# Performance work log

Measured on AMD Instinct MI355X. Metric: run time of the kernel, lower is better.

The kernel has to match this reference:

```python
import jax, jax.numpy as jnp
import numpy as np

B, H, LQ, LK, D = 4, 8, 2048, 2048, 64
FACTOR = 5
SAMPLE_K = min(FACTOR * int(np.ceil(np.log(LK))), LK)  # 40
N_TOP = min(FACTOR * int(np.ceil(np.log(LQ))), LQ)     # 40
SCALE = 1.0 / float(np.sqrt(D))


def setup_inputs() -> dict:
    key = jax.random.key(0)
    kq, kk, kv, ki = jax.random.split(key, 4)
    queries = jax.random.normal(kq, (B, LQ, H, D), dtype=jnp.float32)
    keys = jax.random.normal(kk, (B, LK, H, D), dtype=jnp.float32)
    values = jax.random.normal(kv, (B, LK, H, D), dtype=jnp.float32)
    index_sample = jax.random.randint(ki, (LQ, SAMPLE_K), 0, LK)
    return {"queries": queries, "keys": keys, "values": values,
            "index_sample": index_sample}


def reference(queries, keys, values, index_sample):
    # (B, L, H, D) -> (B, H, L, D)
    Q = queries.transpose(0, 2, 1, 3)
    K = keys.transpose(0, 2, 1, 3)
    V = values.transpose(0, 2, 1, 3)

    # --- _prob_QK: sampled score estimate ---
    # gather sampled keys: (B, H, L_Q, sample_k, D)
    K_sample = K[:, :, index_sample]
    # Q_K_sample: (B, H, L_Q, sample_k)
    qk_sample = jnp.einsum('bhld,bhlsd->bhls', Q, K_sample)
    # sparsity measure M = max - mean over sampled keys
    M = qk_sample.max(axis=-1) - qk_sample.mean(axis=-1)  # (B, H, L_Q)
    _, idx = jax.lax.top_k(M, N_TOP)                      # (B, H, u)

    # exact scores for top queries
    Q_reduce = jnp.take_along_axis(Q, idx[..., None], axis=2)     # (B, H, u, D)
    scores_top = jnp.einsum('bhud,bhkd->bhuk', Q_reduce, K) * SCALE

    # --- initial context (mask_flag=True -> cumulative sum of V) ---
    context = jnp.cumsum(V, axis=2)  # (B, H, L_Q, D)

    # --- update context at top-query positions with exact attention ---
    attn = jax.nn.softmax(scores_top, axis=-1)                    # (B, H, u, L_K)
    context_v = jnp.einsum('bhuk,bhkd->bhud', attn, V)            # (B, H, u, D)
    bi = jnp.arange(B)[:, None, None]
    hi = jnp.arange(H)[None, :, None]
    context = context.at[bi, hi, idx].set(context_v)

    # back to (B, L_Q, H, D); output_attention=False -> attn dropped
    return context.transpose(0, 2, 1, 3)
```

## Files before the change

kernel.cpp:

```cpp
#include <hip/hip_runtime.h>
#include <hip/hip_bf16.h>
#include <math.h>

#define NB 4
#define NH 8
#define SLQ 2048
#define SLK 2048
#define DD 64
#define SK 40
#define NTOP 40
#define SCL 0.125f
#define CH 128
#define NCH (SLK / CH)
#define UB 2
#define NUG (NTOP / UB)
#define NBH (NB * NH)
#define KB 128
#define NKB (SLK / KB)
#define PVU 4
#define NPG (NTOP / PVU)

typedef unsigned short ushort_t;

__device__ __forceinline__ float bf2f(unsigned int u16) {
    union { unsigned int i; float f; } v;
    v.i = u16 << 16;
    return v.f;
}
__device__ __forceinline__ ushort_t f2bf(float f) {
    union { float f; unsigned int i; } v;
    v.f = f;
    unsigned int x = v.i;
    unsigned int r = (x + 0x7FFFu + ((x >> 16) & 1u)) >> 16;
    return (ushort_t)r;
}
template <bool F32>
__device__ __forceinline__ float le(const void* p, size_t i) {
    return F32 ? ((const float*)p)[i] : bf2f(((const ushort_t*)p)[i]);
}
template <bool F32>
__device__ __forceinline__ void se(void* p, size_t i, float v) {
    if (F32) ((float*)p)[i] = v;
    else ((ushort_t*)p)[i] = f2bf(v);
}
template <bool F32>
__device__ __forceinline__ float4 load4(const void* p, size_t off) {
    if (F32) return *(const float4*)((const float*)p + off);
    uint2 u = *(const uint2*)((const ushort_t*)p + off);
    float4 r;
    r.x = bf2f(u.x & 0xffffu); r.y = bf2f(u.x >> 16);
    r.z = bf2f(u.y & 0xffffu); r.w = bf2f(u.y >> 16);
    return r;
}
template <bool F32>
__device__ __forceinline__ void store4(void* p, size_t off, float4 v) {
    if (F32) { *(float4*)((float*)p + off) = v; return; }
    uint2 u;
    u.x = (unsigned)f2bf(v.x) | ((unsigned)f2bf(v.y) << 16);
    u.y = (unsigned)f2bf(v.z) | ((unsigned)f2bf(v.w) << 16);
    *(uint2*)((ushort_t*)p + off) = u;
}
template <bool F32>
__device__ __forceinline__ void load8(const void* p, size_t elem_off, float* r) {
    if (F32) {
        const float4* q = (const float4*)((const float*)p + elem_off);
        float4 a = q[0], b = q[1];
        r[0] = a.x; r[1] = a.y; r[2] = a.z; r[3] = a.w;
        r[4] = b.x; r[5] = b.y; r[6] = b.z; r[7] = b.w;
    } else {
        uint4 u = *(const uint4*)((const ushort_t*)p + elem_off);
        unsigned int w[4] = {u.x, u.y, u.z, u.w};
#pragma unroll
        for (int j = 0; j < 4; j++) {
            r[2 * j + 0] = bf2f(w[j] & 0xffffu);
            r[2 * j + 1] = bf2f(w[j] >> 16);
        }
    }
}

__global__ void k_probe(const unsigned int* __restrict__ qw, int* __restrict__ flag)
{
    int t = threadIdx.x;
    unsigned int w = qw[t * 37];
    int cnt = 0;
#pragma unroll
    for (int s = 0; s < 2; s++) {
        unsigned int h = (s == 0) ? (w & 0xffffu) : (w >> 16);
        unsigned int e = (h >> 7) & 0xffu;
        int ok = (e == 0) ? ((h & 0x7fu) == 0) : (e >= 100 && e <= 153);
        cnt += ok;
    }
#pragma unroll
    for (int off = 32; off > 0; off >>= 1) cnt += __shfl_xor(cnt, off);
    if (t == 0) flag[0] = (cnt >= 104) ? 0 : 1;
}

template <bool F32>
__device__ __forceinline__ void sampleM_body(
    const void* q, const void* k, const int* isamp, float* M)
{
    int t = threadIdx.x;
    int lane = t & 63;
    int blk = blockIdx.x;
    int bh = blk & (NBH - 1);
    int lgrp = blk >> 5;
    int l = lgrp * 4 + (t >> 6);
    int h  = bh & (NH - 1);
    int b  = bh >> 3;
    int sl = lane >> 3, c = lane & 7;

    float q8[8];
    load8<F32>(q, (((size_t)(b * SLQ + l)) * NH + h) * DD + c * 8, q8);
    int il = (lane < SK) ? (isamp[l * SK + lane] & (SLK - 1)) : 0;

    float k8[SK / 8][8];
#pragma unroll
    for (int it = 0; it < SK / 8; it++) {
        int ks = __shfl(il, it * 8 + sl);
        load8<F32>(k, (((size_t)(b * SLK + ks)) * NH + h) * DD + c * 8, k8[it]);
    }
    float dots[SK / 8];
#pragma unroll
    for (int it = 0; it < SK / 8; it++) {
        float dot = 0.f;
#pragma unroll
        for (int j = 0; j < 8; j++) dot += q8[j] * k8[it][j];
        dots[it] = dot;
    }
#pragma unroll
    for (int m = 1; m <= 4; m <<= 1) {
#pragma unroll
        for (int it = 0; it < SK / 8; it++) dots[it] += __shfl_xor(dots[it], m);
    }
    float mx = dots[0], sm = dots[0];
#pragma unroll
    for (int it = 1; it < SK / 8; it++) {
        mx = fmaxf(mx, dots[it]);
        sm += dots[it];
    }
#pragma unroll
    for (int m = 8; m <= 32; m <<= 1) {
        mx = fmaxf(mx, __shfl_xor(mx, m));
        sm += __shfl_xor(sm, m);
    }
    if (lane == 0) M[(size_t)bh * SLQ + l] = mx - sm * (1.0f / SK);
}
__global__ __launch_bounds__(256) void k_sampleM(
    const void* __restrict__ q, const void* __restrict__ k,
    const int* __restrict__ isamp, const int* __restrict__ flag,
    float* __restrict__ M)
{
    if (flag[0]) sampleM_body<true>(q, k, isamp, M);
    else         sampleM_body<false>(q, k, isamp, M);
}

__global__ __launch_bounds__(512) void k_topk(
    const float* __restrict__ M, int* __restrict__ topidx)
{
    int bh = blockIdx.x;
    int t = threadIdx.x;
    int lane = t & 63, wid = t >> 6;
    __shared__ float vals[SLQ];
    __shared__ float wbv[8];
    __shared__ int   wbi[8];
    const float* Mp = M + (size_t)bh * SLQ;
    for (int i = t; i < SLQ; i += 512) vals[i] = Mp[i];
    __syncthreads();
    for (int u = 0; u < NTOP; u++) {
        float bv = -INFINITY; int bi = t & (SLQ - 1);
#pragma unroll
        for (int r = 0; r < SLQ / 512; r++) {
            int i = t + r * 512;
            float v = vals[i];
            if (v > bv) { bv = v; bi = i; }
        }
#pragma unroll
        for (int off = 32; off > 0; off >>= 1) {
            float ov = __shfl_xor(bv, off);
            int   oi = __shfl_xor(bi, off);
            if (ov > bv || (ov == bv && oi < bi)) { bv = ov; bi = oi; }
        }
        if (lane == 0) { wbv[wid] = bv; wbi[wid] = bi; }
        __syncthreads();
        if (t == 0) {
            float fv = wbv[0]; int fi = wbi[0];
#pragma unroll
            for (int w = 1; w < 8; w++) {
                if (wbv[w] > fv || (wbv[w] == fv && wbi[w] < fi)) { fv = wbv[w]; fi = wbi[w]; }
            }
            fi &= (SLQ - 1);
            topidx[bh * NTOP + u] = fi;
            vals[fi] = -INFINITY;
        }
        __syncthreads();
    }
}

template <bool F32>
__device__ __forceinline__ void qk_body(
    const void* q, const void* k, const int* topidx, void* S)
{
    int gid = blockIdx.x;
    int bh = gid & (NBH - 1);
    int kb = gid >> 5;
    int h = bh & 7, b = bh >> 3;
    int t = threadIdx.x;

    __shared__ float Ktd[DD][KB + 4];
    __shared__ float Qs[NTOP][DD + 4];
    __shared__ int lqs[NTOP];

    if (t < NTOP) lqs[t] = topidx[bh * NTOP + t] & (SLQ - 1);
    __syncthreads();

    {
        int r = t >> 1, half = t & 1;
        int key = kb * KB + r;
        size_t base = (((size_t)(b * SLK + key)) * NH + h) * DD + half * 32;
#pragma unroll
        for (int i = 0; i < 8; i++) {
            float4 a = load4<F32>(k, base + i * 4);
            int d0 = half * 32 + i * 4;
            Ktd[d0 + 0][r] = a.x; Ktd[d0 + 1][r] = a.y;
            Ktd[d0 + 2][r] = a.z; Ktd[d0 + 3][r] = a.w;
        }
    }
    for (int lin = t; lin < NTOP * DD / 4; lin += 256) {
        int u = (lin * 4) >> 6, d0 = (lin * 4) & 63;
        float4 a = load4<F32>(q, (((size_t)(b * SLQ + lqs[u])) * NH + h) * DD + d0);
        Qs[u][d0 + 0] = a.x; Qs[u][d0 + 1] = a.y;
        Qs[u][d0 + 2] = a.z; Qs[u][d0 + 3] = a.w;
    }
    __syncthreads();

    int ug = t >> 5;
    int kg = t & 31;
    float4 acc[5];
#pragma unroll
    for (int u = 0; u < 5; u++) acc[u] = {0.f, 0.f, 0.f, 0.f};

#pragma unroll 4
    for (int d4 = 0; d4 < 16; d4++) {
        float4 q4[5];
#pragma unroll
        for (int u = 0; u < 5; u++)
            q4[u] = *(const float4*)&Qs[ug * 5 + u][d4 * 4];
#pragma unroll
        for (int j = 0; j < 4; j++) {
            float4 k4 = *(const float4*)&Ktd[d4 * 4 + j][kg * 4];
            float qs;
#pragma unroll
            for (int u = 0; u < 5; u++) {
                qs = (j == 0) ? q4[u].x : (j == 1) ? q4[u].y : (j == 2) ? q4[u].z : q4[u].w;
                acc[u].x += qs * k4.x; acc[u].y += qs * k4.y;
                acc[u].z += qs * k4.z; acc[u].w += qs * k4.w;
            }
        }
    }
#pragma unroll
    for (int u = 0; u < 5; u++) {
        float4 s4 = {acc[u].x * SCL, acc[u].y * SCL, acc[u].z * SCL, acc[u].w * SCL};
        store4<F32>(S, ((size_t)(bh * NTOP + ug * 5 + u)) * SLK + kb * KB + kg * 4, s4);
    }
}
__global__ __launch_bounds__(256) void k_qk(
    const void* __restrict__ q, const void* __restrict__ k,
    const int* __restrict__ topidx, const int* __restrict__ flag,
    void* __restrict__ S)
{
    if (flag[0]) qk_body<true>(q, k, topidx, S);
    else         qk_body<false>(q, k, topidx, S);
}

template <bool F32>
__device__ __forceinline__ void pv_body(
    const void* S, const void* v, float* ctxv)
{
    int gid = blockIdx.x;
    int bh = gid & (NBH - 1);
    int ug = gid >> 5;
    int h = bh & 7, b = bh >> 3;
    int t = threadIdx.x;
    int lane = t & 63, w = t >> 6;

    __shared__ float sc[PVU][SLK];
    __shared__ float4 part[16][PVU][16];
    __shared__ float dinv[PVU];

    for (int i = 0; i < 8; i++) {
        int lin = (i * 256 + t) * 4;
        int j = lin >> 11, key = lin & (SLK - 1);
        float4 a = load4<F32>(S, ((size_t)(bh * NTOP + ug * PVU + j)) * SLK + key);
        *(float4*)&sc[j][key] = a;
    }
    __syncthreads();

    {
        int j = w;
        float m = -INFINITY;
#pragma unroll
        for (int i = 0; i < 32; i++) m = fmaxf(m, sc[j][i * 64 + lane]);
#pragma unroll
        for (int mm = 1; mm <= 32; mm <<= 1) m = fmaxf(m, __shfl_xor(m, mm));
        float s = 0.f;
#pragma unroll
        for (int i = 0; i < 32; i++) {
            float e = expf(sc[j][i * 64 + lane] - m);
            sc[j][i * 64 + lane] = e;
            s += e;
        }
#pragma unroll
        for (int mm = 1; mm <= 32; mm <<= 1) s += __shfl_xor(s, mm);
        if (lane == 0) dinv[j] = 1.0f / s;
    }
    __syncthreads();

    {
        int d4 = t & 15, rg = t >> 4;
        float4 acc[PVU];
#pragma unroll
        for (int j = 0; j < PVU; j++) acc[j] = {0.f, 0.f, 0.f, 0.f};
        for (int i = 0; i < SLK / 16; i++) {
            int key = rg + i * 16;
            float4 v4 = load4<F32>(v, (((size_t)(b * SLK + key)) * NH + h) * DD + d4 * 4);
#pragma unroll
            for (int j = 0; j < PVU; j++) {
                float sj = sc[j][key];
                acc[j].x += sj * v4.x; acc[j].y += sj * v4.y;
                acc[j].z += sj * v4.z; acc[j].w += sj * v4.w;
            }
        }
#pragma unroll
        for (int j = 0; j < PVU; j++) part[rg][j][d4] = acc[j];
    }
    __syncthreads();
    if (t < 64) {
        int j = t >> 4, d4 = t & 15;
        float4 tot = part[0][j][d4];
#pragma unroll
        for (int rg = 1; rg < 16; rg++) {
            float4 a = part[rg][j][d4];
            tot.x += a.x; tot.y += a.y; tot.z += a.z; tot.w += a.w;
        }
        float di = dinv[j];
        tot.x *= di; tot.y *= di; tot.z *= di; tot.w *= di;
        *(float4*)&ctxv[((size_t)(bh * NTOP + ug * PVU + j)) * DD + d4 * 4] = tot;
    }
}
__global__ __launch_bounds__(256) void k_pv(
    const void* __restrict__ S, const void* __restrict__ v,
    const int* __restrict__ flag, float* __restrict__ ctxv)
{
    if (flag[0]) pv_body<true>(S, v, ctxv);
    else         pv_body<false>(S, v, ctxv);
}

template <bool F32>
__device__ __forceinline__ void scatter_body(
    const float* ctxv, const int* topidx, void* out)
{
    int gid = blockIdx.x;
    int bh = gid & (NBH - 1);
    int ug = gid >> 5;
    int h = bh & 7, b = bh >> 3;
    int t = threadIdx.x;
    int j = t >> 6, d = t & 63;
    int u = ug * PVU + j;
    int lq = topidx[bh * NTOP + u] & (SLQ - 1);
    se<F32>(out, (((size_t)(b * SLQ + lq)) * NH + h) * DD + d,
            ctxv[((size_t)(bh * NTOP + u)) * DD + d]);
}
__global__ __launch_bounds__(256) void k_scatter(
    const float* __restrict__ ctxv, const int* __restrict__ topidx,
    const int* __restrict__ flag, void* __restrict__ out)
{
    if (flag[0]) scatter_body<true>(ctxv, topidx, out);
    else         scatter_body<false>(ctxv, topidx, out);
}

template <bool F32>
__device__ __forceinline__ void csum_body(const void* v, float* bsum)
{
    int gid = blockIdx.x;
    int bh = gid & (NBH - 1);
    int ch = gid >> 5;
    int h = bh & 7, b = bh >> 3;
    int t = threadIdx.x;
    int q4 = t & 15, g = t >> 4;
    int base_row = ch * CH + g * 8;

    float4 s = {0.f, 0.f, 0.f, 0.f};
#pragma unroll
    for (int i = 0; i < 8; i++) {
        float4 a = load4<F32>(v, (((size_t)(b * SLK + base_row + i)) * NH + h) * DD + q4 * 4);
        s.x += a.x; s.y += a.y; s.z += a.z; s.w += a.w;
    }
    __shared__ float4 gs[16][16];
    gs[g][q4] = s;
    __syncthreads();
    if (t < 16) {
        float4 tot = gs[0][t];
#pragma unroll
        for (int g2 = 1; g2 < 16; g2++) {
            tot.x += gs[g2][t].x; tot.y += gs[g2][t].y;
            tot.z += gs[g2][t].z; tot.w += gs[g2][t].w;
        }
        *(float4*)&bsum[((size_t)bh * NCH + ch) * DD + t * 4] = tot;
    }
}
__global__ __launch_bounds__(256) void k_csum(
    const void* __restrict__ v, const int* __restrict__ flag, float* __restrict__ bsum)
{
    if (flag[0]) csum_body<true>(v, bsum);
    else         csum_body<false>(v, bsum);
}

template <bool F32>
__device__ __forceinline__ void scanf_body(const void* v, const float* bsum, void* out)
{
    int gid = blockIdx.x;
    int bh = gid & (NBH - 1);
    int ch = gid >> 5;
    int h = bh & 7, b = bh >> 3;
    int t = threadIdx.x;
    int q4 = t & 15, g = t >> 4;
    int base_row = ch * CH + g * 8;

    float4 pre[8];
    float4 run = {0.f, 0.f, 0.f, 0.f};
#pragma unroll
    for (int i = 0; i < 8; i++) {
        float4 a = load4<F32>(v, (((size_t)(b * SLK + base_row + i)) * NH + h) * DD + q4 * 4);
        run.x += a.x; run.y += a.y; run.z += a.z; run.w += a.w;
        pre[i] = run;
    }
    __shared__ float4 gs[16][16];
    gs[g][q4] = run;
    __syncthreads();

    float4 base = {0.f, 0.f, 0.f, 0.f};
    for (int c = 0; c < ch; c++) {
        float4 a = *(const float4*)&bsum[((size_t)bh * NCH + c) * DD + q4 * 4];
        base.x += a.x; base.y += a.y; base.z += a.z; base.w += a.w;
    }
    for (int g2 = 0; g2 < g; g2++) {
        float4 a = gs[g2][q4];
        base.x += a.x; base.y += a.y; base.z += a.z; base.w += a.w;
    }
#pragma unroll
    for (int i = 0; i < 8; i++) {
        float4 o = {base.x + pre[i].x, base.y + pre[i].y,
                    base.z + pre[i].z, base.w + pre[i].w};
        store4<F32>(out, (((size_t)(b * SLQ + base_row + i)) * NH + h) * DD + q4 * 4, o);
    }
}
__global__ __launch_bounds__(256) void k_scan_fast(
    const void* __restrict__ v, const float* __restrict__ bsum,
    const int* __restrict__ flag, void* __restrict__ out)
{
    if (flag[0]) scanf_body<true>(v, bsum, out);
    else         scanf_body<false>(v, bsum, out);
}

template <bool F32>
__device__ __forceinline__ void scans_body(const void* v, void* out)
{
    int gid = blockIdx.x;
    int bh = gid & (NBH - 1);
    int ch = gid >> 5;
    int h = bh & 7, b = bh >> 3;
    int t = threadIdx.x;
    int q4 = t & 15, g = t >> 4;

    __shared__ float4 pa[16][16];
    __shared__ float4 gs[16][16];

    float4 ps = {0.f, 0.f, 0.f, 0.f};
    int nprior = ch * CH;
    for (int r = g; r < nprior; r += 16) {
        float4 a = load4<F32>(v, (((size_t)(b * SLK + r)) * NH + h) * DD + q4 * 4);
        ps.x += a.x; ps.y += a.y; ps.z += a.z; ps.w += a.w;
    }
    pa[g][q4] = ps;

    int base_row = ch * CH + g * 8;
    float4 pre[8];
    float4 run = {0.f, 0.f, 0.f, 0.f};
#pragma unroll
    for (int i = 0; i < 8; i++) {
        float4 a = load4<F32>(v, (((size_t)(b * SLK + base_row + i)) * NH + h) * DD + q4 * 4);
        run.x += a.x; run.y += a.y; run.z += a.z; run.w += a.w;
        pre[i] = run;
    }
    gs[g][q4] = run;
    __syncthreads();

    float4 base = {0.f, 0.f, 0.f, 0.f};
#pragma unroll
    for (int g2 = 0; g2 < 16; g2++) {
        float4 a = pa[g2][q4];
        base.x += a.x; base.y += a.y; base.z += a.z; base.w += a.w;
    }
    for (int g2 = 0; g2 < g; g2++) {
        float4 a = gs[g2][q4];
        base.x += a.x; base.y += a.y; base.z += a.z; base.w += a.w;
    }
#pragma unroll
    for (int i = 0; i < 8; i++) {
        float4 o = {base.x + pre[i].x, base.y + pre[i].y,
                    base.z + pre[i].z, base.w + pre[i].w};
        store4<F32>(out, (((size_t)(b * SLQ + base_row + i)) * NH + h) * DD + q4 * 4, o);
    }
}
__global__ __launch_bounds__(256) void k_scan_slow(
    const void* __restrict__ v, const int* __restrict__ flag, void* __restrict__ out)
{
    if (flag[0]) scans_body<true>(v, out);
    else         scans_body<false>(v, out);
}

template <bool F32>
__device__ __forceinline__ void attn_body(
    const void* q, const void* k, const void* v,
    const int* topidx, void* out)
{
    int gid = blockIdx.x;
    int bh = gid & (NBH - 1);
    int ug = gid >> 5;
    int h  = bh & 7, b = bh >> 3;
    int t  = threadIdx.x;
    int lane = t & 63, w = t >> 6;
    int sl = lane >> 3, c = lane & 7;

    __shared__ float sc[UB][SLK];
    __shared__ float wred[8][UB];
    __shared__ float gm[UB];
    __shared__ float dinv[UB];
    __shared__ int   lqs[UB];
    __shared__ float part[8][UB][DD];

    if (t < UB) lqs[t] = topidx[bh * NTOP + ug * UB + t] & (SLQ - 1);
    __syncthreads();

    float q8[UB][8];
#pragma unroll
    for (int j = 0; j < UB; j++)
        load8<F32>(q, (((size_t)(b * SLQ + lqs[j])) * NH + h) * DD + c * 8, q8[j]);

#pragma unroll 2
    for (int it = 0; it < 32; it++) {
        int key = w * 256 + it * 8 + sl;
        float k8[8];
        load8<F32>(k, (((size_t)(b * SLK + key)) * NH + h) * DD + c * 8, k8);
#pragma unroll
        for (int j = 0; j < UB; j++) {
            float dot = 0.f;
#pragma unroll
            for (int x = 0; x < 8; x++) dot += q8[j][x] * k8[x];
#pragma unroll
            for (int m = 1; m <= 4; m <<= 1) dot += __shfl_xor(dot, m);
            if (c == j) sc[j][key] = dot * SCL;
        }
    }
    __syncthreads();

#pragma unroll
    for (int j = 0; j < UB; j++) {
        float m = -INFINITY;
#pragma unroll
        for (int i = 0; i < 4; i++) m = fmaxf(m, sc[j][w * 256 + i * 64 + lane]);
#pragma unroll
        for (int mm = 1; mm <= 32; mm <<= 1) m = fmaxf(m, __shfl_xor(m, mm));
        if (lane == 0) wred[w][j] = m;
    }
    __syncthreads();
    if (t < UB) {
        float m = -INFINITY;
#pragma unroll
        for (int w2 = 0; w2 < 8; w2++) m = fmaxf(m, wred[w2][t]);
        gm[t] = m;
    }
    __syncthreads();
#pragma unroll
    for (int j = 0; j < UB; j++) {
        float m = gm[j];
        float s = 0.f;
#pragma unroll
        for (int i = 0; i < 4; i++) {
            int idx = w * 256 + i * 64 + lane;
            float e = expf(sc[j][idx] - m);
            sc[j][idx] = e;
            s += e;
        }
#pragma unroll
        for (int mm = 1; mm <= 32; mm <<= 1) s += __shfl_xor(s, mm);
        if (lane == 0) wred[w][j] = s;
    }
    __syncthreads();
    if (t < UB) {
        float s = 0.f;
#pragma unroll
        for (int w2 = 0; w2 < 8; w2++) s += wred[w2][t];
        dinv[t] = 1.0f / s;
    }
    __syncthreads();

    {
        int l16 = lane & 15, r = lane >> 4;
        float4 acc[UB];
#pragma unroll
        for (int j = 0; j < UB; j++) acc[j] = {0.f, 0.f, 0.f, 0.f};
        for (int i = 0; i < 64; i++) {
            int key = w + (i * 4 + r) * 8;
            float4 v4 = load4<F32>(v, (((size_t)(b * SLK + key)) * NH + h) * DD + l16 * 4);
#pragma unroll
            for (int j = 0; j < UB; j++) {
                float sj = sc[j][key];
                acc[j].x += sj * v4.x; acc[j].y += sj * v4.y;
                acc[j].z += sj * v4.z; acc[j].w += sj * v4.w;
            }
        }
#pragma unroll
        for (int j = 0; j < UB; j++) {
#pragma unroll
            for (int mm = 16; mm <= 32; mm <<= 1) {
                acc[j].x += __shfl_xor(acc[j].x, mm);
                acc[j].y += __shfl_xor(acc[j].y, mm);
                acc[j].z += __shfl_xor(acc[j].z, mm);
                acc[j].w += __shfl_xor(acc[j].w, mm);
            }
            if (r == 0) *(float4*)&part[w][j][l16 * 4] = acc[j];
        }
    }
    __syncthreads();
    if (t < UB * DD) {
        int j = t >> 6, d = t & 63;
        float tot = 0.f;
#pragma unroll
        for (int w2 = 0; w2 < 8; w2++) tot += part[w2][j][d];
        se<F32>(out, (((size_t)(b * SLQ + lqs[j])) * NH + h) * DD + d, tot * dinv[j]);
    }
}
__global__ __launch_bounds__(512) void k_attn(
    const void* __restrict__ q, const void* __restrict__ k,
    const void* __restrict__ v, const int* __restrict__ topidx,
    const int* __restrict__ flag, void* __restrict__ out)
{
    if (flag[0]) attn_body<true>(q, k, v, topidx, out);
    else         attn_body<false>(q, k, v, topidx, out);
}

extern "C" void kernel_launch(void* const* d_in, const int* in_sizes, int n_in,
                              void* d_out, int out_size, void* d_ws, size_t ws_size,
                              hipStream_t stream)
{
    const void* q = d_in[0];
    const void* k = d_in[1];
    const void* v = d_in[2];
    const int* isamp = (const int*)d_in[3];

    int* topidx = (int*)d_ws;
    int* flag   = (int*)((char*)d_ws + 5120);
    float* bsum = (float*)((char*)d_ws + 8192);
    float* ctxv = (float*)((char*)d_ws + 8192 + 131072);
    float* M = (float*)d_out;
    void* S  = d_out;

    const size_t need_fast = 8192 + (size_t)NBH * NCH * DD * 4;
    const size_t need_two  = need_fast + (size_t)NBH * NTOP * DD * 4;
    const bool fast = ws_size >= need_fast;
    const bool two  = ws_size >= need_two;

    k_probe  <<<1,                       64, 0, stream>>>((const unsigned int*)q, flag);
    k_sampleM<<<(NB * NH * SLQ) / 4,    256, 0, stream>>>(q, k, isamp, flag, M);
    k_topk   <<<NBH,                    512, 0, stream>>>(M, topidx);

    if (two) {
        k_qk   <<<NBH * NKB,            256, 0, stream>>>(q, k, topidx, flag, S);
        k_pv   <<<NBH * NPG,            256, 0, stream>>>(S, v, flag, ctxv);
        k_csum     <<<NBH * NCH,        256, 0, stream>>>(v, flag, bsum);
        k_scan_fast<<<NBH * NCH,        256, 0, stream>>>(v, bsum, flag, d_out);
        k_scatter  <<<NBH * NPG,        256, 0, stream>>>(ctxv, topidx, flag, d_out);
    } else {
        if (fast) {
            k_csum     <<<NBH * NCH,    256, 0, stream>>>(v, flag, bsum);
            k_scan_fast<<<NBH * NCH,    256, 0, stream>>>(v, bsum, flag, d_out);
        } else {
            k_scan_slow<<<NBH * NCH,    256, 0, stream>>>(v, flag, d_out);
        }
        k_attn <<<NBH * NUG,            512, 0, stream>>>(q, k, v, topidx, flag, d_out);
    }
}
```

Baseline: 218.9 us.

## Make top-k selection two-level with per-wave register candidates and no block barriers

The top-k kernel used to do 40 rounds of block-wide argmax, each with two __syncthreads and a single-thread final merge over shared memory. Now each wave keeps its 256 values in registers and extracts its own top-40 candidates using only wave shuffles. A single wave then merges the 8x40 candidates with 40 more shuffle-based argmax rounds. This removes the per-round block barriers and serial shared-memory work, but adds a serialized second phase executed by one wave.

```diff
diff --git a/kernel.cpp b/kernel.cpp
--- a/kernel.cpp
+++ b/kernel.cpp
@@ -159,40 +159,64 @@
 {
     int bh = blockIdx.x;
     int t = threadIdx.x;
-    int lane = t & 63, wid = t >> 6;
-    __shared__ float vals[SLQ];
-    __shared__ float wbv[8];
-    __shared__ int   wbi[8];
+    int lane = t & 63, w = t >> 6;
+    __shared__ float cval[8][NTOP];
+    __shared__ int   cidx[8][NTOP];
+
     const float* Mp = M + (size_t)bh * SLQ;
-    for (int i = t; i < SLQ; i += 512) vals[i] = Mp[i];
-    __syncthreads();
+    float v0 = Mp[w * 256 + 0 * 64 + lane];
+    float v1 = Mp[w * 256 + 1 * 64 + lane];
+    float v2 = Mp[w * 256 + 2 * 64 + lane];
+    float v3 = Mp[w * 256 + 3 * 64 + lane];
+
     for (int u = 0; u < NTOP; u++) {
-        float bv = -INFINITY; int bi = t & (SLQ - 1);
-#pragma unroll
-        for (int r = 0; r < SLQ / 512; r++) {
-            int i = t + r * 512;
-            float v = vals[i];
-            if (v > bv) { bv = v; bi = i; }
-        }
-#pragma unroll
-        for (int off = 32; off > 0; off >>= 1) {
+        float bv = v0; int bj = 0;
+        if (v1 > bv) { bv = v1; bj = 1; }
+        if (v2 > bv) { bv = v2; bj = 2; }
+        if (v3 > bv) { bv = v3; bj = 3; }
+        int bi = w * 256 + bj * 64 + lane;
+#pragma unroll
+        for (int off = 1; off <= 32; off <<= 1) {
             float ov = __shfl_xor(bv, off);
             int   oi = __shfl_xor(bi, off);
             if (ov > bv || (ov == bv && oi < bi)) { bv = ov; bi = oi; }
         }
-        if (lane == 0) { wbv[wid] = bv; wbi[wid] = bi; }
-        __syncthreads();
-        if (t == 0) {
-            float fv = wbv[0]; int fi = wbi[0];
-#pragma unroll
-            for (int w = 1; w < 8; w++) {
-                if (wbv[w] > fv || (wbv[w] == fv && wbi[w] < fi)) { fv = wbv[w]; fi = wbi[w]; }
+        int wj = (bi >> 6) & 3, wl = bi & 63;
+        if (lane == wl) {
+            if      (wj == 0) v0 = -INFINITY;
+            else if (wj == 1) v1 = -INFINITY;
+            else if (wj == 2) v2 = -INFINITY;
+            else              v3 = -INFINITY;
+        }
+        if (lane == 0) { cval[w][u] = bv; cidx[w][u] = bi; }
+    }
+    __syncthreads();
+
+    if (w == 0) {
+        float mv[5]; int mi[5];
+#pragma unroll
+        for (int j = 0; j < 5; j++) {
+            int c = lane * 5 + j;
+            mv[j] = cval[c / NTOP][c % NTOP];
+            mi[j] = cidx[c / NTOP][c % NTOP];
+        }
+        for (int u = 0; u < NTOP; u++) {
+            float bv = mv[0]; int bi = mi[0];
+#pragma unroll
+            for (int j = 1; j < 5; j++) {
+                if (mv[j] > bv || (mv[j] == bv && mi[j] < bi)) { bv = mv[j]; bi = mi[j]; }
             }
-            fi &= (SLQ - 1);
-            topidx[bh * NTOP + u] = fi;
-            vals[fi] = -INFINITY;
-        }
-        __syncthreads();
+#pragma unroll
+            for (int off = 1; off <= 32; off <<= 1) {
+                float ov = __shfl_xor(bv, off);
+                int   oi = __shfl_xor(bi, off);
+                if (ov > bv || (ov == bv && oi < bi)) { bv = ov; bi = oi; }
+            }
+#pragma unroll
+            for (int j = 0; j < 5; j++)
+                if (mi[j] == bi) mv[j] = -INFINITY;
+            if (lane == 0) topidx[bh * NTOP + u] = bi & (SLQ - 1);
+        }
     }
 }
 
```

Result: no change. 221.7 us (+1.3%).

## Replace iterative argmax top-k with parallel rank-counting selection

Applied to the files above, without the earlier changes.

The old top-k ran one block per head and did 40 serial argmax passes with two block barriers each. The new version launches 16 blocks per head; each thread computes the rank of one element by comparing it against all 2048 values, exiting early once every lane in the wavefront has rank at least 40. Elements with rank below 40 claim output slots through an atomic counter, which needs a memset before launch. Output order is no longer sorted by score, so downstream kernels must not depend on index order.

```diff
diff --git a/kernel.cpp b/kernel.cpp
--- a/kernel.cpp
+++ b/kernel.cpp
@@ -154,45 +154,38 @@
     else         sampleM_body<false>(q, k, isamp, M);
 }
 
-__global__ __launch_bounds__(512) void k_topk(
-    const float* __restrict__ M, int* __restrict__ topidx)
-{
-    int bh = blockIdx.x;
-    int t = threadIdx.x;
-    int lane = t & 63, wid = t >> 6;
+__global__ __launch_bounds__(128) void k_topk(
+    const float* __restrict__ M, int* __restrict__ topidx, int* __restrict__ cnt)
+{
+    int gid = blockIdx.x;
+    int bh = gid & (NBH - 1);
+    int sb = gid >> 5;
+    int t = threadIdx.x;
     __shared__ float vals[SLQ];
-    __shared__ float wbv[8];
-    __shared__ int   wbi[8];
+
     const float* Mp = M + (size_t)bh * SLQ;
-    for (int i = t; i < SLQ; i += 512) vals[i] = Mp[i];
-    __syncthreads();
-    for (int u = 0; u < NTOP; u++) {
-        float bv = -INFINITY; int bi = t & (SLQ - 1);
-#pragma unroll
-        for (int r = 0; r < SLQ / 512; r++) {
-            int i = t + r * 512;
-            float v = vals[i];
-            if (v > bv) { bv = v; bi = i; }
-        }
-#pragma unroll
-        for (int off = 32; off > 0; off >>= 1) {
-            float ov = __shfl_xor(bv, off);
-            int   oi = __shfl_xor(bi, off);
-            if (ov > bv || (ov == bv && oi < bi)) { bv = ov; bi = oi; }
-        }
-        if (lane == 0) { wbv[wid] = bv; wbi[wid] = bi; }
-        __syncthreads();
-        if (t == 0) {
-            float fv = wbv[0]; int fi = wbi[0];
-#pragma unroll
-            for (int w = 1; w < 8; w++) {
-                if (wbv[w] > fv || (wbv[w] == fv && wbi[w] < fi)) { fv = wbv[w]; fi = wbi[w]; }
-            }
-            fi &= (SLQ - 1);
-            topidx[bh * NTOP + u] = fi;
-            vals[fi] = -INFINITY;
-        }
-        __syncthreads();
+    for (int i = t; i < SLQ / 4; i += 128)
+        ((float4*)vals)[i] = ((const float4*)Mp)[i];
+    __syncthreads();
+
+    int i = sb * 128 + t;
+    float vi = vals[i];
+    int rank = 0;
+    for (int blk = 0; blk < 8; blk++) {
+#pragma unroll 16
+        for (int j4 = blk * 64; j4 < blk * 64 + 64; j4++) {
+            float4 a = ((float4*)vals)[j4];
+            int j = j4 * 4;
+            rank += (a.x > vi || (a.x == vi && (j + 0) < i));
+            rank += (a.y > vi || (a.y == vi && (j + 1) < i));
+            rank += (a.z > vi || (a.z == vi && (j + 2) < i));
+            rank += (a.w > vi || (a.w == vi && (j + 3) < i));
+        }
+        if (__all(rank >= NTOP)) break;
+    }
+    if (rank < NTOP) {
+        int pos = atomicAdd(&cnt[bh], 1);
+        if (pos < NTOP) topidx[bh * NTOP + pos] = i;
     }
 }
 
@@ -661,6 +654,7 @@
 
     int* topidx = (int*)d_ws;
     int* flag   = (int*)((char*)d_ws + 5120);
+    int* cnt    = (int*)((char*)d_ws + 5248);
     float* bsum = (float*)((char*)d_ws + 8192);
     float* ctxv = (float*)((char*)d_ws + 8192 + 131072);
     float* M = (float*)d_out;
@@ -671,9 +665,11 @@
     const bool fast = ws_size >= need_fast;
     const bool two  = ws_size >= need_two;
 
+    hipMemsetAsync(cnt, 0, NBH * sizeof(int), stream);
+
     k_probe  <<<1,                       64, 0, stream>>>((const unsigned int*)q, flag);
     k_sampleM<<<(NB * NH * SLQ) / 4,    256, 0, stream>>>(q, k, isamp, flag, M);
-    k_topk   <<<NBH,                    512, 0, stream>>>(M, topidx);
+    k_topk   <<<NBH * 16,               128, 0, stream>>>(M, topidx, cnt);
 
     if (two) {
         k_qk   <<<NBH * NKB,            256, 0, stream>>>(q, k, topidx, flag, S);
```

After: 235.1 us. 1.07x slower.
